# Kernel tuning notes

Measured on AMD Instinct MI355X. Metric: run time of the kernel, lower is better.

## Reference

```python
import jax, jax.numpy as jnp
import numpy as np

jax.config.update("jax_enable_x64", True)

EPS = 1e-3
MAX_EIG = 1000.0


def setup_inputs() -> dict:
    key = jax.random.key(0)
    a = jax.random.normal(key, (4096, 64, 64), dtype=jnp.float32)
    # symmetrize so input is a valid symmetric matrix (eigvals then clamped to SPD)
    x = 0.5 * (a + jnp.swapaxes(a, -1, -2))
    return {"x": x}


def _clamp_recon(x64, transform):
    # eigh in fp64, clamp eigvals, apply transform, reconstruct V diag(f(w)) V^T
    w, v = jnp.linalg.eigh(x64)
    w = transform(jnp.clip(w, EPS, MAX_EIG))
    return (v * w[..., None, :]) @ jnp.swapaxes(v, -1, -2)


def reference(x) -> jnp.ndarray:
    # safe_eigh: fp64 eigh, clamp eigvals to [eps, max_eig], reconstruct, cast fp32
    x_spd = _clamp_recon(x.astype(jnp.float64), lambda w: w).astype(jnp.float32)
    # matrix log: fp64 eigh again, clamp, log eigvals, reconstruct, cast fp32
    x_log = _clamp_recon(x_spd.astype(jnp.float64), jnp.log).astype(jnp.float32)
    return x_log
```

## Files before the change

kernel.cpp:

```cpp
#include <hip/hip_runtime.h>
#include <math.h>

#define MIN_SWEEPS 6
#define MAX_SWEEPS 9
#define EPSV 1e-3
#define MAXEIG 1000.0
#define EP 68


#define REP64(X) \
  X(0) X(1) X(2) X(3) X(4) X(5) X(6) X(7) \
  X(8) X(9) X(10) X(11) X(12) X(13) X(14) X(15) \
  X(16) X(17) X(18) X(19) X(20) X(21) X(22) X(23) \
  X(24) X(25) X(26) X(27) X(28) X(29) X(30) X(31) \
  X(32) X(33) X(34) X(35) X(36) X(37) X(38) X(39) \
  X(40) X(41) X(42) X(43) X(44) X(45) X(46) X(47) \
  X(48) X(49) X(50) X(51) X(52) X(53) X(54) X(55) \
  X(56) X(57) X(58) X(59) X(60) X(61) X(62) X(63)

__global__ __launch_bounds__(64, 2)
void spd_log_kernel(const float* __restrict__ x, float* __restrict__ out) {
    __shared__ float vlds[64 * EP];

    const int lane = (int)threadIdx.x;
    const size_t mat = blockIdx.x;
    const float* __restrict__ xm = x + mat * (size_t)4096;
    float* __restrict__ om = out + mat * (size_t)4096;

#define DECLW(i) float w##i;
    REP64(DECLW)
#define DECLQ(i) float q##i;
    REP64(DECLQ)

#define LOADW(i) w##i = xm[(i) * 64 + lane];
    REP64(LOADW)

    float ff = 0.0f;
#define ACCF(i) ff = fmaf(w##i, w##i, ff);
    REP64(ACCF)
#pragma unroll
    for (int o = 32; o > 0; o >>= 1) ff += __shfl_xor(ff, o);
    const float gamma = 0.5f * sqrtf(ff);

#define SHIFTW(i) w##i += ((i) == lane) ? gamma : 0.0f;
    REP64(SHIFTW)

    float n = 0.0f;
#define ACCN(i) n = fmaf(w##i, w##i, n);
    REP64(ACCN)

    for (int sweep = 0; sweep < MAX_SWEEPS; ++sweep) {
        n = 0.0f;
        REP64(ACCN)
        float S = n;
#pragma unroll
        for (int o = 32; o > 0; o >>= 1) S += __shfl_xor(S, o);
        float off2 = 0.0f;

        for (int m = 1; m < 64; ++m) {
            const int pidx = ((lane ^ m) << 2);
            float nq;
            asm volatile("ds_bpermute_b32 %0, %1, %2"
                         : "=v"(nq) : "v"(pidx), "v"(n));
#define FETCH(i) asm volatile("ds_bpermute_b32 %0, %1, %2" \
                              : "=v"(q##i) : "v"(pidx), "v"(w##i));
            REP64(FETCH)
            asm volatile("s_waitcnt lgkmcnt(0)");
            __builtin_amdgcn_sched_barrier(0);

            float gp[8] = {0.f, 0.f, 0.f, 0.f, 0.f, 0.f, 0.f, 0.f};
#define ACCG(i) gp[(i) & 7] = fmaf(w##i, q##i, gp[(i) & 7]);
            REP64(ACCG)
            const float g = ((gp[0] + gp[1]) + (gp[2] + gp[3])) +
                            ((gp[4] + gp[5]) + (gp[6] + gp[7]));
            off2 = fmaf(g, g, off2);
            const bool isp = lane < (lane ^ m);
            const float na = isp ? n : nq;
            const float nb = isp ? nq : n;
            const float tau = (nb - na) * (0.5f * __builtin_amdgcn_rcpf(g));
            const float at  = fabsf(tau);
            float t = __builtin_amdgcn_rcpf(at + __builtin_amdgcn_sqrtf(fmaf(at, at, 1.0f)));
            t = copysignf(t, tau);
            float c = __builtin_amdgcn_rsqf(fmaf(t, t, 1.0f));
            float s = t * c;
            const bool tiny = !(fabsf(g) > 1e-28f);
            c = tiny ? 1.0f : c;
            s = tiny ? 0.0f : s;
            const float tg = tiny ? 0.0f : t * g;
            const float se = isp ? -s : s;
#define ROT(i) w##i = fmaf(se, q##i, c * w##i);
            REP64(ROT)
            n += isp ? -tg : tg;
        }
#pragma unroll
        for (int o = 32; o > 0; o >>= 1) off2 += __shfl_xor(off2, o);
        if (sweep >= MIN_SWEEPS - 1 && off2 < 1e-13f * S * S) break;
    }

    n = 0.0f;
    REP64(ACCN)
    const float rn = __builtin_amdgcn_rsqf(n);
#define NRM(i) w##i *= rn;
    REP64(NRM)

#define DUMP(i) vlds[lane * EP + (i)] = w##i;
    REP64(DUMP)
    __syncthreads();

    double acc = 0.0;
    for (int r = 0; r < 64; ++r) {
        double ip[4] = {0.0, 0.0, 0.0, 0.0};
#define RAYI(i) ip[(i) >> 4] = fma((double)xm[r * 64 + (i)], (double)w##i, ip[(i) >> 4]);
        REP64(RAYI)
        const double inner = (ip[0] + ip[1]) + (ip[2] + ip[3]);
        acc = fma((double)vlds[lane * EP + r], inner, acc);
    }
    double lam = fmin(fmax(acc, (double)EPSV), (double)MAXEIG);
    const float f = (float)log(lam);

#define G2(i) q##i = __uint_as_float(__builtin_amdgcn_readlane(__float_as_uint(f), (i))) * vlds[(i) * EP + lane];
    REP64(G2)

    for (int rg = 0; rg < 16; ++rg) {
        const int rg4 = rg * 4;
        float a0 = 0.0f, a1 = 0.0f, a2 = 0.0f, a3 = 0.0f;
#define RECI(i) { const float4 vv = *(const float4*)(vlds + (i) * EP + rg4); \
                  a0 = fmaf(vv.x, q##i, a0); a1 = fmaf(vv.y, q##i, a1);      \
                  a2 = fmaf(vv.z, q##i, a2); a3 = fmaf(vv.w, q##i, a3); }
        REP64(RECI)
        om[(rg4 + 0) * 64 + lane] = a0;
        om[(rg4 + 1) * 64 + lane] = a1;
        om[(rg4 + 2) * 64 + lane] = a2;
        om[(rg4 + 3) * 64 + lane] = a3;
    }
}

extern "C" void kernel_launch(void* const* d_in, const int* in_sizes, int n_in,
                              void* d_out, int out_size, void* d_ws, size_t ws_size,
                              hipStream_t stream) {
    const float* x = (const float*)d_in[0];
    float* out = (float*)d_out;
    const int nmat = in_sizes[0] / 4096;
    spd_log_kernel<<<dim3(nmat), dim3(64), 0, stream>>>(x, out);
}
```

Baseline: 1.667 ms.

## Halve LDS footprint by staging eigenvectors in two passes

Shrinks the shared eigenvector buffer from 64 to 32 rows. The Rayleigh-quotient step now loads the eigenvector matrix in two halves, and the reconstruction runs as two passes that accumulate into global output. The aim is to lower per-block LDS so more blocks can be resident per CU. In exchange it adds extra barriers, a second global read-modify-write pass over the output, and reconstruction split into two partial sums.

```diff
diff --git a/kernel.cpp b/kernel.cpp
--- a/kernel.cpp
+++ b/kernel.cpp
@@ -18,11 +18,19 @@
   X(48) X(49) X(50) X(51) X(52) X(53) X(54) X(55) \
   X(56) X(57) X(58) X(59) X(60) X(61) X(62) X(63)
 
+#define REP32(X) \
+  X(0) X(1) X(2) X(3) X(4) X(5) X(6) X(7) \
+  X(8) X(9) X(10) X(11) X(12) X(13) X(14) X(15) \
+  X(16) X(17) X(18) X(19) X(20) X(21) X(22) X(23) \
+  X(24) X(25) X(26) X(27) X(28) X(29) X(30) X(31)
+
 __global__ __launch_bounds__(64, 2)
 void spd_log_kernel(const float* __restrict__ x, float* __restrict__ out) {
-    __shared__ float vlds[64 * EP];
+    __shared__ float vlds[32 * EP];
 
     const int lane = (int)threadIdx.x;
+    const int hb   = lane >> 5;
+    const int rl   = lane & 31;
     const size_t mat = blockIdx.x;
     const float* __restrict__ xm = x + mat * (size_t)4096;
     float* __restrict__ om = out + mat * (size_t)4096;
@@ -103,35 +111,62 @@
 #define NRM(i) w##i *= rn;
     REP64(NRM)
 
-#define DUMP(i) vlds[lane * EP + (i)] = w##i;
-    REP64(DUMP)
+    double acc = 0.0;
+#define DUMPA0(i) if ((i) < 32) vlds[(i) * 64 + lane] = w##i;
+    REP64(DUMPA0)
     __syncthreads();
-
-    double acc = 0.0;
-    for (int r = 0; r < 64; ++r) {
+    for (int r = 0; r < 32; ++r) {
         double ip[4] = {0.0, 0.0, 0.0, 0.0};
 #define RAYI(i) ip[(i) >> 4] = fma((double)xm[r * 64 + (i)], (double)w##i, ip[(i) >> 4]);
         REP64(RAYI)
         const double inner = (ip[0] + ip[1]) + (ip[2] + ip[3]);
-        acc = fma((double)vlds[lane * EP + r], inner, acc);
+        acc = fma((double)vlds[r * 64 + lane], inner, acc);
     }
+    __syncthreads();
+#define DUMPA1(i) if ((i) >= 32) vlds[((i) - 32) * 64 + lane] = w##i;
+    REP64(DUMPA1)
+    __syncthreads();
+    for (int r = 32; r < 64; ++r) {
+        double ip[4] = {0.0, 0.0, 0.0, 0.0};
+        REP64(RAYI)
+        const double inner = (ip[0] + ip[1]) + (ip[2] + ip[3]);
+        acc = fma((double)vlds[(r - 32) * 64 + lane], inner, acc);
+    }
+
     double lam = fmin(fmax(acc, (double)EPSV), (double)MAXEIG);
     const float f = (float)log(lam);
 
-#define G2(i) q##i = __uint_as_float(__builtin_amdgcn_readlane(__float_as_uint(f), (i))) * vlds[(i) * EP + lane];
-    REP64(G2)
+#pragma unroll
+    for (int P = 0; P < 2; ++P) {
+        __syncthreads();
+        if (hb == P) {
+#define DUMPB(i) vlds[rl * EP + (i)] = w##i;
+            REP64(DUMPB)
+        }
+        __syncthreads();
 
-    for (int rg = 0; rg < 16; ++rg) {
-        const int rg4 = rg * 4;
-        float a0 = 0.0f, a1 = 0.0f, a2 = 0.0f, a3 = 0.0f;
+#define G2(i) q##i = __uint_as_float(__builtin_amdgcn_readlane(__float_as_uint(f), 32 * P + (i))) * vlds[(i) * EP + lane];
+        REP32(G2)
+
+        for (int rg = 0; rg < 16; ++rg) {
+            const int rg4 = rg * 4;
+            float a0 = 0.0f, a1 = 0.0f, a2 = 0.0f, a3 = 0.0f;
 #define RECI(i) { const float4 vv = *(const float4*)(vlds + (i) * EP + rg4); \
                   a0 = fmaf(vv.x, q##i, a0); a1 = fmaf(vv.y, q##i, a1);      \
                   a2 = fmaf(vv.z, q##i, a2); a3 = fmaf(vv.w, q##i, a3); }
-        REP64(RECI)
-        om[(rg4 + 0) * 64 + lane] = a0;
-        om[(rg4 + 1) * 64 + lane] = a1;
-        om[(rg4 + 2) * 64 + lane] = a2;
-        om[(rg4 + 3) * 64 + lane] = a3;
+            REP32(RECI)
+            if (P == 0) {
+                om[(rg4 + 0) * 64 + lane] = a0;
+                om[(rg4 + 1) * 64 + lane] = a1;
+                om[(rg4 + 2) * 64 + lane] = a2;
+                om[(rg4 + 3) * 64 + lane] = a3;
+            } else {
+                om[(rg4 + 0) * 64 + lane] += a0;
+                om[(rg4 + 1) * 64 + lane] += a1;
+                om[(rg4 + 2) * 64 + lane] += a2;
+                om[(rg4 + 3) * 64 + lane] += a3;
+            }
+        }
     }
 }
 
```

Result: no change. 1.657 ms (-0.6%).
